# Optimization experiments

Hardware: AMD Instinct MI355X
Metric: run time of the kernel (lower is better)

The kernel has to match this reference:

```python
import jax, jax.numpy as jnp
import numpy as np

DIM = 2048
N_HEADS = 16
KV_HEADS = 2 * 2  # 4
HEAD_DIM = DIM // N_HEADS  # 128
B, T = 2, 2048


def apply_rope(x, cos, sin):
    # Faithful to the source: x is replaced by its rotated version, then
    # multiplied by (sin + cos). x: [B,H,T,D], cos/sin: [T,D] broadcast.
    x1 = x[..., ::2]
    x2 = x[..., 1::2]
    rot = jnp.stack((-x2, x1), axis=-1).reshape(x.shape)
    return rot * sin + rot * cos


def setup_inputs() -> dict:
    key = jax.random.key(0)
    ks = jax.random.split(key, 8)
    x = jax.random.normal(ks[0], (B, T, DIM), dtype=jnp.float32)
    cos = jax.random.uniform(ks[1], (T, HEAD_DIM), dtype=jnp.float32)
    sin = jax.random.uniform(ks[2], (T, HEAD_DIM), dtype=jnp.float32)
    mask = jnp.tril(jnp.ones((T, T), dtype=bool))  # causal
    s = 1.0 / np.sqrt(DIM)
    Wq = jax.random.normal(ks[3], (DIM, DIM), dtype=jnp.float32) * s
    Wk = jax.random.normal(ks[4], (KV_HEADS * HEAD_DIM, DIM), dtype=jnp.float32) * s
    Wv = jax.random.normal(ks[5], (KV_HEADS * HEAD_DIM, DIM), dtype=jnp.float32) * s
    Wout = jax.random.normal(ks[6], (DIM, DIM), dtype=jnp.float32) * s
    bout = jax.random.normal(ks[7], (DIM,), dtype=jnp.float32) * s
    return {"x": x, "cos": cos, "sin": sin, "mask": mask,
            "Wq": Wq, "Wk": Wk, "Wv": Wv, "Wout": Wout, "bout": bout}


def reference(x, cos, sin, mask, Wq, Wk, Wv, Wout, bout):
    Bb, Tt, C = x.shape
    # projections (torch Linear: x @ W.T)
    q = (x @ Wq.T).reshape(Bb, Tt, N_HEADS, HEAD_DIM).transpose(0, 2, 1, 3)
    k = (x @ Wk.T).reshape(Bb, Tt, KV_HEADS, HEAD_DIM).transpose(0, 2, 1, 3)
    v = (x @ Wv.T).reshape(Bb, Tt, KV_HEADS, HEAD_DIM).transpose(0, 2, 1, 3)
    q = apply_rope(q, cos, sin)
    k = apply_rope(k, cos, sin)
    repeat = N_HEADS // KV_HEADS
    k = jnp.repeat(k, repeat, axis=1)  # [B,H,T,D]
    v = jnp.repeat(v, repeat, axis=1)
    attn = jnp.einsum("bhtd,bhsd->bhts", q, k) / np.sqrt(HEAD_DIM)
    attn = jnp.where(mask, attn, jnp.float32(-1e9))
    probs = jax.nn.softmax(attn, axis=-1)
    out = jnp.einsum("bhts,bhsd->bhtd", probs, v)
    out = out.transpose(0, 2, 1, 3).reshape(Bb, Tt, C)
    return out @ Wout.T + bout
```

## Files before the change

kernel.cpp:

```cpp
#include <hip/hip_runtime.h>
#include <type_traits>

#define DEVI __device__ __forceinline__

typedef unsigned short u16;
typedef unsigned int u32;
typedef float f32x4 __attribute__((ext_vector_type(4)));
typedef __bf16 bf16x8 __attribute__((ext_vector_type(8)));
typedef unsigned short u16x4 __attribute__((ext_vector_type(4)));
typedef unsigned short u16x8 __attribute__((ext_vector_type(8)));
typedef int i32x4 __attribute__((ext_vector_type(4)));
typedef unsigned int u32x2 __attribute__((ext_vector_type(2)));

constexpr int BATCH = 2;
constexpr int T     = 2048;
constexpr int DIM   = 2048;
constexpr int NH    = 16;
constexpr int KVH   = 4;
constexpr int HD    = 128;
constexpr int NQKV  = DIM + 2 * KVH * HD;
constexpr int ROWS  = BATCH * T;
constexpr float SCALE = 0.08838834764831845f;
constexpr float SC2   = 0.08838834764831845f * 1.4426950408889634f;

DEVI u16 f2b(float f) {
  u32 u = __float_as_uint(f);
  return (u16)((u + 0x7fffu + ((u >> 16) & 1u)) >> 16);
}
DEVI float b2f(u16 u) { return __uint_as_float(((u32)u) << 16); }

DEVI u32 cvtpk(float lo, float hi) {
  u32 r;
  asm("v_cvt_pk_bf16_f32 %0, %1, %2" : "=v"(r) : "v"(lo), "v"(hi));
  return r;
}

DEVI f32x4 mfma16(bf16x8 a, bf16x8 b, f32x4 c) {
  return __builtin_amdgcn_mfma_f32_16x16x32_bf16(a, b, c, 0, 0, 0);
}
DEVI void gload16(const void* g, void* l) {
  __builtin_amdgcn_global_load_lds((const __attribute__((address_space(1))) void*)g,
                                   (__attribute__((address_space(3))) void*)l, 16, 0, 0);
}

__global__ void cvt_bf16_kernel(const float* __restrict__ in, u16* __restrict__ out, int n4) {
  int i = blockIdx.x * 256 + threadIdx.x;
  if (i >= n4) return;
  float4 v = *((const float4*)in + i);
  u16x4 o = { f2b(v.x), f2b(v.y), f2b(v.z), f2b(v.w) };
  *((u16x4*)out + i) = o;
}

__global__ void cs_kernel(const float* __restrict__ c, const float* __restrict__ s,
                          float* __restrict__ cs, int n) {
  int i = blockIdx.x * 256 + threadIdx.x;
  if (i < n) cs[i] = c[i] + s[i];
}

template<bool BF16OUT, bool BIAS>
__global__ __launch_bounds__(256) void gemm_bt_kernel(
    const u16* __restrict__ A, const u16* __restrict__ W,
    void* __restrict__ Cout, const float* __restrict__ bias,
    int M, int N, int K)
{
  constexpr int BK = 64;
  __shared__ u16 sA[128 * BK];
  __shared__ u16 sB[128 * BK];
  const int nbx = N >> 7;
  const int bx = blockIdx.x % nbx;
  const int by = blockIdx.x / nbx;
  const int m0 = by << 7, n0 = bx << 7;
  const int tid = threadIdx.x;
  const int w = tid >> 6, lane = tid & 63;
  const int wr = w >> 1, wc = w & 1;
  const int lq = lane & 15, lg = lane >> 4;

  f32x4 acc[4][4] = {};

  int srow[4], scb[4];
#pragma unroll
  for (int c = 0; c < 4; ++c) {
    int off = (w * 4 + c) * 1024 + lane * 16;
    srow[c] = off >> 7;
    scb[c]  = (off & 127) ^ ((srow[c] & 7) << 4);
  }

  for (int kt = 0; kt < K; kt += BK) {
#pragma unroll
    for (int c = 0; c < 4; ++c) {
      u16* la = sA + (w * 4 + c) * 512;
      u16* lb = sB + (w * 4 + c) * 512;
      gload16(A + (size_t)(m0 + srow[c]) * K + kt + (scb[c] >> 1), la);
      gload16(W + (size_t)(n0 + srow[c]) * K + kt + (scb[c] >> 1), lb);
    }
    __syncthreads();
#pragma unroll
    for (int ks = 0; ks < 2; ++ks) {
      bf16x8 af[4], bfr[4];
#pragma unroll
      for (int i = 0; i < 4; ++i) {
        int ra = wr * 64 + i * 16 + lq;
        int ca = (ks * 64 + lg * 16) ^ ((ra & 7) << 4);
        af[i] = *(const bf16x8*)((const char*)sA + ra * 128 + ca);
        int rb = wc * 64 + i * 16 + lq;
        int cb = (ks * 64 + lg * 16) ^ ((rb & 7) << 4);
        bfr[i] = *(const bf16x8*)((const char*)sB + rb * 128 + cb);
      }
#pragma unroll
      for (int i = 0; i < 4; ++i)
#pragma unroll
        for (int j = 0; j < 4; ++j)
          acc[i][j] = mfma16(af[i], bfr[j], acc[i][j]);
    }
    __syncthreads();
  }

  const int crow = m0 + wr * 64 + lg * 4;
  const int ccol = n0 + wc * 64 + lq;
#pragma unroll
  for (int j = 0; j < 4; ++j) {
    int col = ccol + j * 16;
    float bv = BIAS ? bias[col] : 0.0f;
#pragma unroll
    for (int i = 0; i < 4; ++i)
#pragma unroll
      for (int r = 0; r < 4; ++r) {
        size_t idx = (size_t)(crow + i * 16 + r) * N + col;
        float v = acc[i][j][r] + bv;
        if (BF16OUT) ((u16*)Cout)[idx] = f2b(v);
        else         ((float*)Cout)[idx] = v;
      }
  }
}

template<int NHEADS, int COLBASE>
__global__ void rope_kernel(const u16* __restrict__ Y, const float* __restrict__ cs,
                            u16* __restrict__ out, float scale)
{
  int pid = blockIdx.x * 256 + threadIdx.x;
  constexpr int TOTAL = ROWS * NHEADS * (HD / 2);
  if (pid >= TOTAL) return;
  int i  = pid & 63;
  int hr = pid >> 6;
  int h  = hr & (NHEADS - 1);
  int r  = hr / NHEADS;
  int t  = r & (T - 1);
  int b  = r >> 11;
  u32 y = *(const u32*)(Y + (size_t)r * NQKV + COLBASE + h * HD + 2 * i);
  float y0 = b2f((u16)(y & 0xffffu));
  float y1 = b2f((u16)(y >> 16));
  const float* cp = cs + t * HD + 2 * i;
  u32 o = (u32)f2b(-y1 * cp[0] * scale) | ((u32)f2b(y0 * cp[1] * scale) << 16);
  *(u32*)(out + (((size_t)(b * NHEADS + h) * T + t) * HD + 2 * i)) = o;
}

__global__ __launch_bounds__(256) void vt_kernel(const u16* __restrict__ Y, u16* __restrict__ vt)
{
  __shared__ u16 tile[64][136];
  const int tid = threadIdx.x;
  const int tc = blockIdx.x & 31;
  const int kh = (blockIdx.x >> 5) & 3;
  const int b  = blockIdx.x >> 7;
  const u16* src = Y + (size_t)(b * T + tc * 64) * NQKV + (DIM + KVH * HD) + kh * HD;
#pragma unroll
  for (int pass = 0; pass < 4; ++pass) {
    int r = pass * 16 + (tid >> 4);
    int c = (tid & 15) * 8;
    *(u16x8*)&tile[r][c] = *(const u16x8*)(src + (size_t)r * NQKV + c);
  }
  __syncthreads();
  const int d = tid >> 1, th = tid & 1;
  u16* dst = vt + ((size_t)((b * KVH + kh) * HD + d) * T) + tc * 64 + th * 32;
#pragma unroll
  for (int j = 0; j < 4; ++j) {
    u16x8 v;
#pragma unroll
    for (int e = 0; e < 8; ++e) v[e] = tile[th * 32 + j * 8 + e][d];
    *(u16x8*)(dst + j * 8) = v;
  }
}

__global__ __launch_bounds__(256, 2) void attn_kernel(
    const u16* __restrict__ Qr, const u16* __restrict__ Kr,
    const u16* __restrict__ Vt, u16* __restrict__ Aout)
{
  __shared__ u16 ldsK[2][64 * 128];
  __shared__ u16 ldsV[2][128 * 64];
  __shared__ u16 ldsP[4][32 * 40];

  const int tid = threadIdx.x;
  const int w = tid >> 6, lane = tid & 63;
  const int lq = lane & 15, lg = lane >> 4;

  const int bh = blockIdx.x >> 4;
  const int p  = blockIdx.x & 15;
  const int b = bh >> 4, h = bh & 15, kh = h >> 2;
  const int qcA = p, qcB = 31 - p;
  const int rowA = qcA * 64 + w * 16;
  const int rowB = qcB * 64 + w * 16;
  const int nst = qcB + 1;

  bf16x8 qf[2][4];
  {
    const u16* QpA = Qr + ((size_t)bh * T + rowA + lq) * HD + lg * 8;
    const u16* QpB = Qr + ((size_t)bh * T + rowB + lq) * HD + lg * 8;
#pragma unroll
    for (int ds = 0; ds < 4; ++ds) {
      qf[0][ds] = *(const bf16x8*)(QpA + ds * 32);
      qf[1][ds] = *(const bf16x8*)(QpB + ds * 32);
    }
  }

  const u16* Kg = Kr + (size_t)(b * KVH + kh) * T * HD;
  const u16* Vg = Vt + (size_t)(b * KVH + kh) * HD * T;

  int kgo[4], klb[4], vgo[4], vlb[4];
  {
    const int vr = lane >> 3, vc = lane & 7;
#pragma unroll
    for (int i = 0; i < 4; ++i) {
      int krow = w * 16 + i * 4 + lg;
      kgo[i] = krow * HD + (((lq * 16) ^ ((krow & 7) << 4)) >> 1);
      klb[i] = (w * 16 + i * 4) * 128;
      int vrow = w * 32 + i * 8 + vr;
      vgo[i] = vrow * T + (((vc * 16) ^ ((vr & 7) << 4)) >> 1);
      vlb[i] = (w * 32 + i * 8) * 64;
    }
  }

  f32x4 accO[2][8] = {};
  float m[2]    = { -1e30f, -1e30f };
  float lsum[2] = { 0.f, 0.f };

#pragma unroll
  for (int i = 0; i < 4; ++i) {
    gload16(Kg + kgo[i], &ldsK[0][klb[i]]);
    gload16(Vg + vgo[i], &ldsV[0][vlb[i]]);
  }
  __syncthreads();

  int cur = 0;
  for (int t = 0; t < nst; ++t) {
    if (t + 1 < nst) {
      const u16* Kt  = Kg + (size_t)(t + 1) * 64 * HD;
      const u16* Vts = Vg + (t + 1) * 64;
#pragma unroll
      for (int i = 0; i < 4; ++i) {
        gload16(Kt + kgo[i],  &ldsK[cur ^ 1][klb[i]]);
        gload16(Vts + vgo[i], &ldsV[cur ^ 1][vlb[i]]);
      }
    }
    const int s0 = t << 6;
    const u16* Kb = ldsK[cur];
    const u16* Vb = ldsV[cur];

    auto softmax_qg = [&](f32x4 (&s4)[4], int qidx, bool diag, float& mm, float& ls,
                          f32x4 (&aO)[8], float (&pp)[16]) {
      float pm = -1e30f;
      if (diag) {
#pragma unroll
        for (int si = 0; si < 4; ++si)
#pragma unroll
          for (int r = 0; r < 4; ++r) {
            int s = s0 + si * 16 + lg * 4 + r;
            float v = (s <= qidx) ? s4[si][r] : -1e9f;
            pp[si * 4 + r] = v; pm = fmaxf(pm, v);
          }
      } else {
#pragma unroll
        for (int si = 0; si < 4; ++si)
#pragma unroll
          for (int r = 0; r < 4; ++r) {
            float v = s4[si][r];
            pp[si * 4 + r] = v; pm = fmaxf(pm, v);
          }
      }
      pm = fmaxf(pm, __shfl_xor(pm, 16));
      pm = fmaxf(pm, __shfl_xor(pm, 32));
      if (!__all(pm <= mm + 11.5f)) {
        float mn = fmaxf(mm, pm);
        float al = __builtin_amdgcn_exp2f(mm - mn);
        mm = mn; ls *= al;
#pragma unroll
        for (int db = 0; db < 8; ++db) aO[db] *= al;
      }
      float ps = 0.f;
#pragma unroll
      for (int i2 = 0; i2 < 16; ++i2) {
        float e = __builtin_amdgcn_exp2f(pp[i2] - mm);
        pp[i2] = e; ps += e;
      }
      ps += __shfl_xor(ps, 16);
      ps += __shfl_xor(ps, 32);
      ls += ps;
    };

    auto tile_body = [&](auto hasA_c) {
      constexpr bool HASA = decltype(hasA_c)::value;
      f32x4 aS[2][4] = {};
      __builtin_amdgcn_s_setprio(1);
#pragma unroll
      for (int si = 0; si < 4; ++si)
#pragma unroll
        for (int ds = 0; ds < 4; ++ds) {
          const u16* kp = Kb + (si * 16 + lq) * 128 +
                          (((ds * 64 + lg * 16) ^ ((lq & 7) << 4)) >> 1);
          bf16x8 kf = *(const bf16x8*)kp;
          if constexpr (HASA) aS[0][si] = mfma16(kf, qf[0][ds], aS[0][si]);
          aS[1][si] = mfma16(kf, qf[1][ds], aS[1][si]);
        }
      __builtin_amdgcn_s_setprio(0);

      float pp[2][16];
      if constexpr (HASA)
        softmax_qg(aS[0], rowA + lq, t == qcA, m[0], lsum[0], accO[0], pp[0]);
      softmax_qg(aS[1], rowB + lq, t == qcB, m[1], lsum[1], accO[1], pp[1]);

#pragma unroll
      for (int ks = 0; ks < 2; ++ks) {
        if constexpr (HASA) {
          u16* pw = &ldsP[w][lq * 40];
          u32x2 wa = { cvtpk(pp[0][8 * ks + 0], pp[0][8 * ks + 1]),
                       cvtpk(pp[0][8 * ks + 2], pp[0][8 * ks + 3]) };
          u32x2 wb = { cvtpk(pp[0][8 * ks + 4], pp[0][8 * ks + 5]),
                       cvtpk(pp[0][8 * ks + 6], pp[0][8 * ks + 7]) };
          *(u32x2*)(pw + lg * 4)      = wa;
          *(u32x2*)(pw + 16 + lg * 4) = wb;
        }
        {
          u16* pw = &ldsP[w][(16 + lq) * 40];
          u32x2 wa = { cvtpk(pp[1][8 * ks + 0], pp[1][8 * ks + 1]),
                       cvtpk(pp[1][8 * ks + 2], pp[1][8 * ks + 3]) };
          u32x2 wb = { cvtpk(pp[1][8 * ks + 4], pp[1][8 * ks + 5]),
                       cvtpk(pp[1][8 * ks + 6], pp[1][8 * ks + 7]) };
          *(u32x2*)(pw + lg * 4)      = wa;
          *(u32x2*)(pw + 16 + lg * 4) = wb;
        }
        asm volatile("" ::: "memory");
        bf16x8 pf0, pf1;
        if constexpr (HASA) pf0 = *(const bf16x8*)(&ldsP[w][lq * 40] + lg * 8);
        pf1 = *(const bf16x8*)(&ldsP[w][(16 + lq) * 40] + lg * 8);
        asm volatile("" ::: "memory");
        __builtin_amdgcn_s_setprio(1);
#pragma unroll
        for (int db = 0; db < 8; ++db) {
          const u16* vp = Vb + (db * 16 + lq) * 64 +
                          (((ks * 64 + lg * 16) ^ ((lq & 7) << 4)) >> 1);
          bf16x8 vf = *(const bf16x8*)vp;
          if constexpr (HASA) accO[0][db] = mfma16(vf, pf0, accO[0][db]);
          accO[1][db] = mfma16(vf, pf1, accO[1][db]);
        }
        __builtin_amdgcn_s_setprio(0);
      }
    };

    if (t <= qcA) tile_body(std::integral_constant<bool, true>{});
    else          tile_body(std::integral_constant<bool, false>{});

    __syncthreads();
    cur ^= 1;
  }

#pragma unroll
  for (int qg = 0; qg < 2; ++qg) {
    const int rowX = qg ? rowB : rowA;
    float inv = 1.0f / (qg ? lsum[1] : lsum[0]);
    u16* Ab = Aout + ((size_t)b * T + rowX + lq) * DIM + h * HD;
#pragma unroll
    for (int db = 0; db < 8; ++db) {
      f32x4 a = qg ? accO[1][db] : accO[0][db];
      u32x2 st = { cvtpk(a[0] * inv, a[1] * inv),
                   cvtpk(a[2] * inv, a[3] * inv) };
      *(u32x2*)(Ab + db * 16 + lg * 4) = st;
    }
  }
}

extern "C" void kernel_launch(void* const* d_in, const int* in_sizes, int n_in,
                              void* d_out, int out_size, void* d_ws, size_t ws_size,
                              hipStream_t stream) {
  const float* x    = (const float*)d_in[0];
  const float* cosp = (const float*)d_in[1];
  const float* sinp = (const float*)d_in[2];
  const float* Wq   = (const float*)d_in[4];
  const float* Wk   = (const float*)d_in[5];
  const float* Wv   = (const float*)d_in[6];
  const float* Wo   = (const float*)d_in[7];
  const float* bo   = (const float*)d_in[8];

  char* ws = (char*)d_ws;
  u16*   xb   = (u16*)(ws + 0);
  u16*   wqkv = (u16*)(ws + 16777216);
  u16*   wout = (u16*)(ws + 29360128);
  float* cs   = (float*)(ws + 37748736);
  u16*   yqkv = (u16*)(ws + 38797312);
  u16*   kr   = (u16*)(ws + 63963136);
  u16*   vt   = (u16*)(ws + 68157440);
  u16* qr   = xb;
  u16* aout = yqkv;

  cvt_bf16_kernel<<<ROWS * DIM / 4 / 256, 256, 0, stream>>>(x, xb, ROWS * DIM / 4);
  cvt_bf16_kernel<<<DIM * DIM / 4 / 256, 256, 0, stream>>>(Wq, wqkv, DIM * DIM / 4);
  cvt_bf16_kernel<<<512 * DIM / 4 / 256, 256, 0, stream>>>(Wk, wqkv + DIM * DIM, 512 * DIM / 4);
  cvt_bf16_kernel<<<512 * DIM / 4 / 256, 256, 0, stream>>>(Wv, wqkv + (size_t)(DIM + 512) * DIM, 512 * DIM / 4);
  cvt_bf16_kernel<<<DIM * DIM / 4 / 256, 256, 0, stream>>>(Wo, wout, DIM * DIM / 4);
  cs_kernel<<<T * HD / 256, 256, 0, stream>>>(cosp, sinp, cs, T * HD);

  gemm_bt_kernel<true, false><<<(ROWS / 128) * (NQKV / 128), 256, 0, stream>>>(
      xb, wqkv, yqkv, nullptr, ROWS, NQKV, DIM);

  rope_kernel<NH, 0><<<ROWS * NH * 64 / 256, 256, 0, stream>>>(yqkv, cs, qr, SC2);
  rope_kernel<KVH, DIM><<<ROWS * KVH * 64 / 256, 256, 0, stream>>>(yqkv, cs, kr, 1.0f);
  vt_kernel<<<BATCH * KVH * (T / 64), 256, 0, stream>>>(yqkv, vt);

  attn_kernel<<<BATCH * NH * 16, 256, 0, stream>>>(qr, kr, vt, aout);

  gemm_bt_kernel<false, true><<<(ROWS / 128) * (DIM / 128), 256, 0, stream>>>(
      aout, wout, d_out, bo, ROWS, DIM, DIM);
}
```

Measured before the change: 223.1 us.

## Replace GEMM with 8-wave triple-buffered pipelined kernel and fuse conversion launches

```diff
diff --git a/kernel.cpp b/kernel.cpp
--- a/kernel.cpp
+++ b/kernel.cpp
@@ -43,90 +43,170 @@
                                    (__attribute__((address_space(3))) void*)l, 16, 0, 0);
 }
 
-__global__ void cvt_bf16_kernel(const float* __restrict__ in, u16* __restrict__ out, int n4) {
+__global__ void cvt_all_kernel(const float* __restrict__ x,
+                               const float* __restrict__ Wq, const float* __restrict__ Wk,
+                               const float* __restrict__ Wv, const float* __restrict__ Wo,
+                               const float* __restrict__ cosp, const float* __restrict__ sinp,
+                               u16* __restrict__ xb, u16* __restrict__ wqkv,
+                               u16* __restrict__ wout, float* __restrict__ cs)
+{
+  constexpr int S0 = ROWS * DIM / 4;
+  constexpr int S1 = DIM * DIM / 4;
+  constexpr int S2 = 512 * DIM / 4;
+  constexpr int S3 = 512 * DIM / 4;
+  constexpr int S4 = DIM * DIM / 4;
+  constexpr int S5 = T * HD / 4;
   int i = blockIdx.x * 256 + threadIdx.x;
-  if (i >= n4) return;
-  float4 v = *((const float4*)in + i);
+  const float* src; u16* dst;
+  if (i < S0) { src = x; dst = xb; }
+  else if ((i -= S0) < S1) { src = Wq; dst = wqkv; }
+  else if ((i -= S1) < S2) { src = Wk; dst = wqkv + DIM * DIM; }
+  else if ((i -= S2) < S3) { src = Wv; dst = wqkv + (size_t)(DIM + 512) * DIM; }
+  else if ((i -= S3) < S4) { src = Wo; dst = wout; }
+  else if ((i -= S4) < S5) {
+    float4 c = ((const float4*)cosp)[i];
+    float4 s = ((const float4*)sinp)[i];
+    float4 o = { c.x + s.x, c.y + s.y, c.z + s.z, c.w + s.w };
+    ((float4*)cs)[i] = o;
+    return;
+  } else return;
+  float4 v = ((const float4*)src)[i];
   u16x4 o = { f2b(v.x), f2b(v.y), f2b(v.z), f2b(v.w) };
-  *((u16x4*)out + i) = o;
-}
-
-__global__ void cs_kernel(const float* __restrict__ c, const float* __restrict__ s,
-                          float* __restrict__ cs, int n) {
-  int i = blockIdx.x * 256 + threadIdx.x;
-  if (i < n) cs[i] = c[i] + s[i];
+  ((u16x4*)dst)[i] = o;
 }
 
 template<bool BF16OUT, bool BIAS>
-__global__ __launch_bounds__(256) void gemm_bt_kernel(
+__global__ __launch_bounds__(512, 2) void gemm8_kernel(
     const u16* __restrict__ A, const u16* __restrict__ W,
     void* __restrict__ Cout, const float* __restrict__ bias,
     int M, int N, int K)
 {
-  constexpr int BK = 64;
-  __shared__ u16 sA[128 * BK];
-  __shared__ u16 sB[128 * BK];
+  __shared__ u16 sA[3][256 * 64];
+  __shared__ u16 sB[3][128 * 64];
+  const int tid = threadIdx.x;
+  const int wid = tid >> 6, lane = tid & 63;
+  const int wr = wid >> 2, wc = wid & 3;
+  const int lq = lane & 15, lg = lane >> 4;
+
   const int nbx = N >> 7;
-  const int bx = blockIdx.x % nbx;
-  const int by = blockIdx.x / nbx;
-  const int m0 = by << 7, n0 = bx << 7;
-  const int tid = threadIdx.x;
-  const int w = tid >> 6, lane = tid & 63;
-  const int wr = w >> 1, wc = w & 1;
-  const int lq = lane & 15, lg = lane >> 4;
-
-  f32x4 acc[4][4] = {};
-
-  int srow[4], scb[4];
-#pragma unroll
-  for (int c = 0; c < 4; ++c) {
-    int off = (w * 4 + c) * 1024 + lane * 16;
-    srow[c] = off >> 7;
-    scb[c]  = (off & 127) ^ ((srow[c] & 7) << 4);
-  }
-
-  for (int kt = 0; kt < K; kt += BK) {
-#pragma unroll
-    for (int c = 0; c < 4; ++c) {
-      u16* la = sA + (w * 4 + c) * 512;
-      u16* lb = sB + (w * 4 + c) * 512;
-      gload16(A + (size_t)(m0 + srow[c]) * K + kt + (scb[c] >> 1), la);
-      gload16(W + (size_t)(n0 + srow[c]) * K + kt + (scb[c] >> 1), lb);
-    }
-    __syncthreads();
-#pragma unroll
-    for (int ks = 0; ks < 2; ++ks) {
-      bf16x8 af[4], bfr[4];
-#pragma unroll
-      for (int i = 0; i < 4; ++i) {
-        int ra = wr * 64 + i * 16 + lq;
-        int ca = (ks * 64 + lg * 16) ^ ((ra & 7) << 4);
-        af[i] = *(const bf16x8*)((const char*)sA + ra * 128 + ca);
-        int rb = wc * 64 + i * 16 + lq;
-        int cb = (ks * 64 + lg * 16) ^ ((rb & 7) << 4);
-        bfr[i] = *(const bf16x8*)((const char*)sB + rb * 128 + cb);
-      }
-#pragma unroll
-      for (int i = 0; i < 4; ++i)
-#pragma unroll
-        for (int j = 0; j < 4; ++j)
-          acc[i][j] = mfma16(af[i], bfr[j], acc[i][j]);
-    }
-    __syncthreads();
-  }
-
-  const int crow = m0 + wr * 64 + lg * 4;
-  const int ccol = n0 + wc * 64 + lq;
-#pragma unroll
-  for (int j = 0; j < 4; ++j) {
-    int col = ccol + j * 16;
+  const int cpx = gridDim.x >> 3;
+  const int swz = (blockIdx.x & 7) * cpx + (blockIdx.x >> 3);
+  const int by = swz / nbx, bx = swz - by * nbx;
+  const int m0 = by << 8, n0 = bx << 7;
+
+  const int srow = wid * 8 + (lane >> 3);
+  const int scol = (((lane & 7) * 16) ^ ((srow & 7) << 4)) >> 1;
+  size_t aoff[4]; int aldst[4];
+#pragma unroll
+  for (int i = 0; i < 4; ++i) {
+    aoff[i] = (size_t)(m0 + i * 64 + srow) * K + scol;
+    aldst[i] = (i * 64 + wid * 8) * 64;
+  }
+  size_t boff[2]; int bldst[2];
+#pragma unroll
+  for (int i = 0; i < 2; ++i) {
+    boff[i] = (size_t)(n0 + i * 64 + srow) * K + scol;
+    bldst[i] = (i * 64 + wid * 8) * 64;
+  }
+
+  const int abase = (wr * 128 + lq) * 128;
+  const int bbase = (wc * 32 + lq) * 128;
+  int cks[2];
+#pragma unroll
+  for (int ks = 0; ks < 2; ++ks) cks[ks] = (ks * 64 + lg * 16) ^ ((lq & 7) << 4);
+
+  f32x4 acc[8][2] = {};
+
+#pragma unroll
+  for (int i = 0; i < 4; ++i) gload16(A + aoff[i], &sA[0][aldst[i]]);
+#pragma unroll
+  for (int i = 0; i < 2; ++i) gload16(W + boff[i], &sB[0][bldst[i]]);
+#pragma unroll
+  for (int i = 0; i < 4; ++i) gload16(A + aoff[i] + 64, &sA[1][aldst[i]]);
+#pragma unroll
+  for (int i = 0; i < 2; ++i) gload16(W + boff[i] + 64, &sB[1][bldst[i]]);
+  asm volatile("s_waitcnt vmcnt(6)" ::: "memory");
+  __builtin_amdgcn_s_barrier();
+
+  const int NT = K >> 6;
+  int cur = 0, pre = 2;
+  for (int t = 0; t < NT; ++t) {
+    const u16* Ap = A + (size_t)(t + 2) * 64;
+    const u16* Wp = W + (size_t)(t + 2) * 64;
+    const bool st = (t + 2 < NT);
+    const char* sAc = (const char*)sA[cur];
+    const char* sBc = (const char*)sB[cur];
+    u16* sAp = sA[pre];
+    u16* sBp = sB[pre];
+
+    bf16x8 bF[2][2], aF[2][2];
+
+#define LDA_PH(Q)                                                              \
+    _Pragma("unroll")                                                          \
+    for (int mm = 0; mm < 2; ++mm)                                             \
+      _Pragma("unroll")                                                        \
+      for (int ks = 0; ks < 2; ++ks)                                           \
+        aF[mm][ks] = *(const bf16x8*)(sAc + abase + (2 * (Q) + mm) * 2048 + cks[ks]);
+
+#define MFMA_PH(Q)                                                             \
+    __builtin_amdgcn_s_setprio(1);                                             \
+    _Pragma("unroll")                                                          \
+    for (int mm = 0; mm < 2; ++mm)                                             \
+      _Pragma("unroll")                                                        \
+      for (int fn = 0; fn < 2; ++fn)                                           \
+        _Pragma("unroll")                                                      \
+        for (int ks = 0; ks < 2; ++ks)                                         \
+          acc[2 * (Q) + mm][fn] = mfma16(aF[mm][ks], bF[fn][ks], acc[2 * (Q) + mm][fn]); \
+    __builtin_amdgcn_s_setprio(0);
+
+    if (st) { gload16(Ap + aoff[0], sAp + aldst[0]); gload16(Ap + aoff[1], sAp + aldst[1]); }
+#pragma unroll
+    for (int fn = 0; fn < 2; ++fn)
+#pragma unroll
+      for (int ks = 0; ks < 2; ++ks)
+        bF[fn][ks] = *(const bf16x8*)(sBc + bbase + fn * 2048 + cks[ks]);
+    LDA_PH(0)
+    __builtin_amdgcn_s_barrier();
+    MFMA_PH(0)
+    __builtin_amdgcn_s_barrier();
+
+    if (st) { gload16(Ap + aoff[2], sAp + aldst[2]); gload16(Ap + aoff[3], sAp + aldst[3]); }
+    LDA_PH(1)
+    __builtin_amdgcn_s_barrier();
+    MFMA_PH(1)
+    __builtin_amdgcn_s_barrier();
+
+    if (st) { gload16(Wp + boff[0], sBp + bldst[0]); gload16(Wp + boff[1], sBp + bldst[1]); }
+    LDA_PH(2)
+    __builtin_amdgcn_s_barrier();
+    MFMA_PH(2)
+    __builtin_amdgcn_s_barrier();
+
+    LDA_PH(3)
+    __builtin_amdgcn_s_barrier();
+    MFMA_PH(3)
+    if (st)                 asm volatile("s_waitcnt vmcnt(6)" ::: "memory");
+    else if (t + 1 < NT)    asm volatile("s_waitcnt vmcnt(0)" ::: "memory");
+    __builtin_amdgcn_s_barrier();
+
+#undef LDA_PH
+#undef MFMA_PH
+    cur = (cur == 2) ? 0 : cur + 1;
+    pre = (pre == 2) ? 0 : pre + 1;
+  }
+
+  const int crow = m0 + wr * 128 + lg * 4;
+  const int ccol = n0 + wc * 32 + lq;
+#pragma unroll
+  for (int fn = 0; fn < 2; ++fn) {
+    int col = ccol + fn * 16;
     float bv = BIAS ? bias[col] : 0.0f;
 #pragma unroll
-    for (int i = 0; i < 4; ++i)
+    for (int fm = 0; fm < 8; ++fm)
 #pragma unroll
       for (int r = 0; r < 4; ++r) {
-        size_t idx = (size_t)(crow + i * 16 + r) * N + col;
-        float v = acc[i][j][r] + bv;
+        size_t idx = (size_t)(crow + fm * 16 + r) * N + col;
+        float v = acc[fm][fn][r] + bv;
         if (BF16OUT) ((u16*)Cout)[idx] = f2b(v);
         else         ((float*)Cout)[idx] = v;
       }
@@ -399,14 +479,12 @@
   u16* qr   = xb;
   u16* aout = yqkv;
 
-  cvt_bf16_kernel<<<ROWS * DIM / 4 / 256, 256, 0, stream>>>(x, xb, ROWS * DIM / 4);
-  cvt_bf16_kernel<<<DIM * DIM / 4 / 256, 256, 0, stream>>>(Wq, wqkv, DIM * DIM / 4);
-  cvt_bf16_kernel<<<512 * DIM / 4 / 256, 256, 0, stream>>>(Wk, wqkv + DIM * DIM, 512 * DIM / 4);
-  cvt_bf16_kernel<<<512 * DIM / 4 / 256, 256, 0, stream>>>(Wv, wqkv + (size_t)(DIM + 512) * DIM, 512 * DIM / 4);
-  cvt_bf16_kernel<<<DIM * DIM / 4 / 256, 256, 0, stream>>>(Wo, wout, DIM * DIM / 4);
-  cs_kernel<<<T * HD / 256, 256, 0, stream>>>(cosp, sinp, cs, T * HD);
-
-  gemm_bt_kernel<true, false><<<(ROWS / 128) * (NQKV / 128), 256, 0, stream>>>(
+  constexpr int CVT_TOTAL = ROWS * DIM / 4 + DIM * DIM / 4 + 512 * DIM / 4 * 2
+                          + DIM * DIM / 4 + T * HD / 4;
+  cvt_all_kernel<<<(CVT_TOTAL + 255) / 256, 256, 0, stream>>>(
+      x, Wq, Wk, Wv, Wo, cosp, sinp, xb, wqkv, wout, cs);
+
+  gemm8_kernel<true, false><<<(ROWS / 256) * (NQKV / 128), 512, 0, stream>>>(
       xb, wqkv, yqkv, nullptr, ROWS, NQKV, DIM);
 
   rope_kernel<NH, 0><<<ROWS * NH * 64 / 256, 256, 0, stream>>>(yqkv, cs, qr, SC2);
@@ -415,6 +493,6 @@
 
   attn_kernel<<<BATCH * NH * 16, 256, 0, stream>>>(qr, kr, vt, aout);
 
-  gemm_bt_kernel<false, true><<<(ROWS / 128) * (DIM / 128), 256, 0, stream>>>(
+  gemm8_kernel<false, true><<<(ROWS / 256) * (DIM / 128), 512, 0, stream>>>(
       aout, wout, d_out, bo, ROWS, DIM, DIM);
 }
```

Measured after the change: 277.6 us. 24.5% more time.
